# Kernel tuning notes

Hardware: AMD Instinct MI355X
Metric: run time of the kernel (lower is better)

Reference implementation:

```python
import jax, jax.numpy as jnp
import numpy as np

OBJ_DIM, REL_DIM, EFF_DIM = 3, 1, 1
REL_HID, OBJ_HID = 150, 100
B, N, E = 4, 2048, 8192
N_RECUR = 1


def _linear_init(k, fan_in, fan_out):
    s = 1.0 / np.sqrt(fan_in)
    k1, k2 = jax.random.split(k)
    W = jax.random.uniform(k1, (fan_in, fan_out), jnp.float32, -s, s)
    b = jax.random.uniform(k2, (fan_out,), jnp.float32, -s, s)
    return W, b


def setup_inputs() -> dict:
    key = jax.random.key(0)
    ks = jax.random.split(key, 9)
    objects = jax.random.normal(ks[0], (B, N, OBJ_DIM), jnp.float32)
    # one-hot incidence matrices [B, N, E]: column e selects sender/receiver node of edge e
    snd_idx = jax.random.randint(ks[1], (B, E), 0, N)
    rcv_idx = jax.random.randint(ks[2], (B, E), 0, N)
    sender_relations = jax.nn.one_hot(snd_idx, N, dtype=jnp.float32).transpose(0, 2, 1)
    receiver_relations = jax.nn.one_hot(rcv_idx, N, dtype=jnp.float32).transpose(0, 2, 1)
    relation_info = jax.random.normal(ks[3], (B, REL_DIM, E), jnp.float32)
    rW1, rb1 = _linear_init(ks[4], 2 * OBJ_DIM + REL_DIM, REL_HID)
    rW2, rb2 = _linear_init(ks[5], REL_HID, REL_HID)
    rW3, rb3 = _linear_init(ks[6], REL_HID, EFF_DIM)
    oW1, ob1 = _linear_init(ks[7], OBJ_DIM + EFF_DIM, OBJ_HID)
    oW2, ob2 = _linear_init(ks[8], OBJ_HID, OBJ_DIM)
    return dict(objects=objects, sender_relations=sender_relations,
                receiver_relations=receiver_relations, relation_info=relation_info,
                rW1=rW1, rb1=rb1, rW2=rW2, rb2=rb2, rW3=rW3, rb3=rb3,
                oW1=oW1, ob1=ob1, oW2=oW2, ob2=ob2)


def _relational(x, rW1, rb1, rW2, rb2, rW3, rb3):
    # per-edge MLP: [B, E, 2*obj+rel] -> [B, E, eff], sigmoid head (edge weight)
    h = jax.nn.relu(x @ rW1 + rb1)
    h = jax.nn.relu(h @ rW2 + rb2)
    return jax.nn.sigmoid(h @ rW3 + rb3)


def _object(x, oW1, ob1, oW2, ob2):
    # per-node MLP: [B, N, obj+eff] -> [B, N, obj]
    h = jax.nn.relu(x @ oW1 + ob1)
    return h @ oW2 + ob2


def reference(objects, sender_relations, receiver_relations, relation_info,
              rW1, rb1, rW2, rb2, rW3, rb3, oW1, ob1, oW2, ob2):
    obj = objects                                   # [B, N, D]
    rel_t = relation_info.transpose(0, 2, 1)        # [B, E, REL_DIM]
    for _ in range(N_RECUR):
        # gather via dense one-hot matmul (faithful to torch.matmul(obj.t(), S))
        snd = jnp.einsum('bnd,bne->bed', obj, sender_relations)
        rcv = jnp.einsum('bnd,bne->bed', obj, receiver_relations)
        inter = jnp.concatenate([snd, rcv, rel_t], axis=-1)      # [B, E, 2D+rel]
        eff = _relational(inter, rW1, rb1, rW2, rb2, rW3, rb3)   # [B, E, eff]
        eff_rcv = jnp.einsum('bne,bef->bnf', receiver_relations, eff)  # scatter-add to nodes
        agg = jnp.concatenate([obj, eff_rcv], axis=-1)           # [B, N, D+eff]
        obj = _object(agg, oW1, ob1, oW2, ob2)
    snd = jnp.einsum('bnd,bne->bed', obj, sender_relations)
    rcv = jnp.einsum('bnd,bne->bed', obj, receiver_relations)
    inter = jnp.concatenate([snd, rcv, rel_t], axis=-1)
    edge_weights = _relational(inter, rW1, rb1, rW2, rb2, rW3, rb3)  # [B, E, eff]
    return edge_weights
```

## Files before the change

kernel.cpp:

```cpp
#include <hip/hip_runtime.h>

#define BB 4
#define NN 2048
#define EE 8192
#define RH 150
#define RHP 152
#define LSTR 156
#define OH 100
#define JPW 19

typedef float f4_t __attribute__((ext_vector_type(4)));

__global__ __launch_bounds__(256) void extract_idx2_kernel(
    const float* __restrict__ S, const float* __restrict__ R,
    int* __restrict__ snd_idx, int* __restrict__ rcv_idx)
{
    const bool second = blockIdx.x >= 2048;
    const float* __restrict__ M = second ? R : S;
    int* __restrict__ idx = second ? rcv_idx : snd_idx;

    const unsigned total4 = (unsigned)BB * NN * EE / 4u;
    unsigned i = (blockIdx.x & 2047u) * 256u + threadIdx.x;
    const unsigned stride = 2048u * 256u;
    for (; i < total4; i += stride) {
        const f4_t v = __builtin_nontemporal_load(reinterpret_cast<const f4_t*>(M) + i);
        if (v.x > 0.5f || v.y > 0.5f || v.z > 0.5f || v.w > 0.5f) {
            const unsigned flat = i * 4u;
            const unsigned e = flat & (EE - 1u);
            const unsigned n = (flat >> 13) & (NN - 1u);
            const unsigned b = flat >> 24;
            if (v.x > 0.5f) idx[b * EE + e + 0u] = (int)n;
            if (v.y > 0.5f) idx[b * EE + e + 1u] = (int)n;
            if (v.z > 0.5f) idx[b * EE + e + 2u] = (int)n;
            if (v.w > 0.5f) idx[b * EE + e + 3u] = (int)n;
        }
    }
}

__global__ void pad_weights_kernel(const float* __restrict__ W2, const float* __restrict__ b2,
                                   const float* __restrict__ W3,
                                   float* __restrict__ W2p, float* __restrict__ b2p,
                                   float* __restrict__ W3p) {
    const int t = blockIdx.x * 256 + (int)threadIdx.x;
    if (t < RHP * RHP) {
        const int k = t / RHP, j = t - k * RHP;
        W2p[t] = (k < RH && j < RH) ? W2[k * RH + j] : 0.0f;
    }
    if (t < RHP) {
        b2p[t] = (t < RH) ? b2[t] : 0.0f;
        W3p[t] = (t < RH) ? W3[t] : 0.0f;
    }
}

template <int PASS>
__global__ __launch_bounds__(512) void edge_mlp_v3(
    const float* __restrict__ obj,
    const int* __restrict__ snd_idx, const int* __restrict__ rcv_idx,
    const float* __restrict__ rel,
    const float* __restrict__ W1, const float* __restrict__ b1,
    const float* __restrict__ W2p, const float* __restrict__ b2p,
    const float* __restrict__ W3p, const float* __restrict__ b3,
    float* __restrict__ out)
{
    __shared__ float h1s[64 * LSTR];
    __shared__ float red[512];

    const int t = (int)threadIdx.x;
    const int ebase = (int)blockIdx.x * 64;
    const int e = t & 63;
    const int jg = t >> 6;
    const int eg = ebase + e;
    const int b = eg >> 13;

    float x[7];
    {
        const int sn = snd_idx[eg];
        const int rn = rcv_idx[eg];
        const float* ps = obj + ((b << 11) + sn) * 3;
        const float* pr = obj + ((b << 11) + rn) * 3;
        x[0] = ps[0]; x[1] = ps[1]; x[2] = ps[2];
        x[3] = pr[0]; x[4] = pr[1]; x[5] = pr[2];
        x[6] = rel[eg];
    }

    for (int j = jg; j < LSTR; j += 8) {
        float v = 0.0f;
        if (j < RH) {
            v = b1[j];
#pragma unroll
            for (int k = 0; k < 7; ++k) v = fmaf(x[k], W1[k * RH + j], v);
            v = fmaxf(v, 0.0f);
        }
        h1s[e * LSTR + j] = v;
    }
    __syncthreads();

    const int w = __builtin_amdgcn_readfirstlane(jg);
    const int jbase = w * JPW;

    float acc[JPW];
#pragma unroll
    for (int m = 0; m < JPW; ++m) acc[m] = b2p[jbase + m];

    const float* hrow = h1s + e * LSTR;
    for (int kc = 0; kc < RHP; kc += 4) {
        const float4 hv = *reinterpret_cast<const float4*>(hrow + kc);
        const float* r0 = W2p + (kc + 0) * RHP + jbase;
        const float* r1 = r0 + RHP;
        const float* r2 = r1 + RHP;
        const float* r3 = r2 + RHP;
#pragma unroll
        for (int m = 0; m < JPW; ++m) {
            float a = acc[m];
            a = fmaf(hv.x, r0[m], a);
            a = fmaf(hv.y, r1[m], a);
            a = fmaf(hv.z, r2[m], a);
            a = fmaf(hv.w, r3[m], a);
            acc[m] = a;
        }
    }

    float o = 0.0f;
#pragma unroll
    for (int m = 0; m < JPW; ++m)
        o = fmaf(fmaxf(acc[m], 0.0f), W3p[jbase + m], o);

    red[t] = o;
    __syncthreads();

    if (t < 64) {
        float tot = b3[0];
#pragma unroll
        for (int i = 0; i < 8; ++i) tot += red[t + 64 * i];
        const float eff = 1.0f / (1.0f + __expf(-tot));
        if (PASS == 0) atomicAdd(&out[(b << 11) + rcv_idx[eg]], eff);
        else           out[eg] = eff;
    }
}

__global__ void object_mlp_kernel(
    const float* __restrict__ obj, const float* __restrict__ eff_rcv,
    const float* __restrict__ W1, const float* __restrict__ b1,
    const float* __restrict__ W2, const float* __restrict__ b2,
    float* __restrict__ obj_new)
{
    const int t = blockIdx.x * blockDim.x + (int)threadIdx.x;
    if (t >= BB * NN) return;
    const float x0 = obj[t * 3 + 0];
    const float x1 = obj[t * 3 + 1];
    const float x2 = obj[t * 3 + 2];
    const float x3 = eff_rcv[t];
    float a0 = b2[0], a1 = b2[1], a2 = b2[2];
#pragma unroll
    for (int j = 0; j < OH; ++j) {
        float h = b1[j];
        h = fmaf(x0, W1[0 * OH + j], h);
        h = fmaf(x1, W1[1 * OH + j], h);
        h = fmaf(x2, W1[2 * OH + j], h);
        h = fmaf(x3, W1[3 * OH + j], h);
        h = fmaxf(h, 0.0f);
        a0 = fmaf(h, W2[j * 3 + 0], a0);
        a1 = fmaf(h, W2[j * 3 + 1], a1);
        a2 = fmaf(h, W2[j * 3 + 2], a2);
    }
    obj_new[t * 3 + 0] = a0;
    obj_new[t * 3 + 1] = a1;
    obj_new[t * 3 + 2] = a2;
}

extern "C" void kernel_launch(void* const* d_in, const int* in_sizes, int n_in,
                              void* d_out, int out_size, void* d_ws, size_t ws_size,
                              hipStream_t stream) {
    (void)in_sizes; (void)n_in; (void)out_size; (void)ws_size;

    const float* objects = (const float*)d_in[0];
    const float* S       = (const float*)d_in[1];
    const float* R       = (const float*)d_in[2];
    const float* rel     = (const float*)d_in[3];
    const float* rW1     = (const float*)d_in[4];
    const float* rb1     = (const float*)d_in[5];
    const float* rW2     = (const float*)d_in[6];
    const float* rb2     = (const float*)d_in[7];
    const float* rW3     = (const float*)d_in[8];
    const float* rb3     = (const float*)d_in[9];
    const float* oW1     = (const float*)d_in[10];
    const float* ob1     = (const float*)d_in[11];
    const float* oW2     = (const float*)d_in[12];
    const float* ob2     = (const float*)d_in[13];

    char* ws = (char*)d_ws;
    int*   snd_idx = (int*)(ws + 0);
    int*   rcv_idx = (int*)(ws + (128 << 10));
    float* eff_rcv = (float*)(ws + (256 << 10));
    float* obj_new = (float*)(ws + (288 << 10));
    float* W2p     = (float*)(ws + (384 << 10));
    float* b2p     = (float*)(ws + (480 << 10));
    float* W3p     = (float*)(ws + (481 << 10));

    extract_idx2_kernel<<<4096, 256, 0, stream>>>(S, R, snd_idx, rcv_idx);

    pad_weights_kernel<<<(RHP * RHP + 255) / 256, 256, 0, stream>>>(
        rW2, rb2, rW3, W2p, b2p, W3p);
    hipMemsetAsync(eff_rcv, 0, BB * NN * sizeof(float), stream);

    edge_mlp_v3<0><<<(BB * EE) / 64, 512, 0, stream>>>(
        objects, snd_idx, rcv_idx, rel, rW1, rb1, W2p, b2p, W3p, rb3, eff_rcv);

    object_mlp_kernel<<<(BB * NN + 255) / 256, 256, 0, stream>>>(
        objects, eff_rcv, oW1, ob1, oW2, ob2, obj_new);

    edge_mlp_v3<1><<<(BB * EE) / 64, 512, 0, stream>>>(
        obj_new, snd_idx, rcv_idx, rel, rW1, rb1, W2p, b2p, W3p, rb3, (float*)d_out);
}
```

Measured before the change: 140.7 us.

## Fuse weight padding into index scan and object MLP into second edge pass

Merges the weight padding and eff_rcv zeroing into the index-extraction kernel, which removes a kernel launch and a memset. The object MLP is folded into the second edge kernel: each block recomputes the updated node features for the 128 sender and receiver nodes its edges touch, so the separate object kernel and its global round trip go away. The cost is redundant object-MLP work, since nodes referenced by many edges get recomputed in several blocks, and 128 threads run a serial 100-step loop while the rest of the block waits.

```diff
diff --git a/kernel.cpp b/kernel.cpp
--- a/kernel.cpp
+++ b/kernel.cpp
@@ -11,10 +11,26 @@
 
 typedef float f4_t __attribute__((ext_vector_type(4)));
 
-__global__ __launch_bounds__(256) void extract_idx2_kernel(
+__global__ __launch_bounds__(256) void scan_prep_kernel(
     const float* __restrict__ S, const float* __restrict__ R,
-    int* __restrict__ snd_idx, int* __restrict__ rcv_idx)
-{
+    const float* __restrict__ rW2, const float* __restrict__ rb2,
+    const float* __restrict__ rW3,
+    int* __restrict__ snd_idx, int* __restrict__ rcv_idx,
+    float* __restrict__ W2p, float* __restrict__ b2p, float* __restrict__ W3p,
+    float* __restrict__ eff_rcv)
+{
+    const unsigned gtid = blockIdx.x * 256u + threadIdx.x;
+
+    if (gtid < RHP * RHP) {
+        const int k = (int)gtid / RHP, j = (int)gtid - k * RHP;
+        W2p[gtid] = (k < RH && j < RH) ? rW2[k * RH + j] : 0.0f;
+    }
+    if (gtid < RHP) {
+        b2p[gtid] = (gtid < RH) ? rb2[gtid] : 0.0f;
+        W3p[gtid] = (gtid < RH) ? rW3[gtid] : 0.0f;
+    }
+    if (gtid < BB * NN) eff_rcv[gtid] = 0.0f;
+
     const bool second = blockIdx.x >= 2048;
     const float* __restrict__ M = second ? R : S;
     int* __restrict__ idx = second ? rcv_idx : snd_idx;
@@ -37,30 +53,72 @@
     }
 }
 
-__global__ void pad_weights_kernel(const float* __restrict__ W2, const float* __restrict__ b2,
-                                   const float* __restrict__ W3,
-                                   float* __restrict__ W2p, float* __restrict__ b2p,
-                                   float* __restrict__ W3p) {
-    const int t = blockIdx.x * 256 + (int)threadIdx.x;
-    if (t < RHP * RHP) {
-        const int k = t / RHP, j = t - k * RHP;
-        W2p[t] = (k < RH && j < RH) ? W2[k * RH + j] : 0.0f;
-    }
-    if (t < RHP) {
-        b2p[t] = (t < RH) ? b2[t] : 0.0f;
-        W3p[t] = (t < RH) ? W3[t] : 0.0f;
-    }
-}
-
-template <int PASS>
-__global__ __launch_bounds__(512) void edge_mlp_v3(
+__device__ __forceinline__ float edge_mlp_body(
+    const float x[7], int t, int e, int jg,
+    const float* __restrict__ W1, const float* __restrict__ b1,
+    const float* __restrict__ W2p, const float* __restrict__ b2p,
+    const float* __restrict__ W3p, const float* __restrict__ b3,
+    float* __restrict__ h1s, float* __restrict__ red)
+{
+    for (int j = jg; j < LSTR; j += 8) {
+        float v = 0.0f;
+        if (j < RH) {
+            v = b1[j];
+#pragma unroll
+            for (int k = 0; k < 7; ++k) v = fmaf(x[k], W1[k * RH + j], v);
+            v = fmaxf(v, 0.0f);
+        }
+        h1s[e * LSTR + j] = v;
+    }
+    __syncthreads();
+
+    const int w = __builtin_amdgcn_readfirstlane(jg);
+    const int jbase = w * JPW;
+
+    float acc[JPW];
+#pragma unroll
+    for (int m = 0; m < JPW; ++m) acc[m] = b2p[jbase + m];
+
+    const float* hrow = h1s + e * LSTR;
+    for (int kc = 0; kc < RHP; kc += 4) {
+        const float4 hv = *reinterpret_cast<const float4*>(hrow + kc);
+        const float* r0 = W2p + (kc + 0) * RHP + jbase;
+        const float* r1 = r0 + RHP;
+        const float* r2 = r1 + RHP;
+        const float* r3 = r2 + RHP;
+#pragma unroll
+        for (int m = 0; m < JPW; ++m) {
+            float a = acc[m];
+            a = fmaf(hv.x, r0[m], a);
+            a = fmaf(hv.y, r1[m], a);
+            a = fmaf(hv.z, r2[m], a);
+            a = fmaf(hv.w, r3[m], a);
+            acc[m] = a;
+        }
+    }
+
+    float o = 0.0f;
+#pragma unroll
+    for (int m = 0; m < JPW; ++m)
+        o = fmaf(fmaxf(acc[m], 0.0f), W3p[jbase + m], o);
+
+    red[t] = o;
+    __syncthreads();
+
+    float tot = b3[0];
+#pragma unroll
+    for (int i = 0; i < 8; ++i) tot += red[(t & 63) + 64 * i];
+    return 1.0f / (1.0f + __expf(-tot));
+}
+
+__global__ __launch_bounds__(512) void edge0_kernel(
     const float* __restrict__ obj,
     const int* __restrict__ snd_idx, const int* __restrict__ rcv_idx,
     const float* __restrict__ rel,
     const float* __restrict__ W1, const float* __restrict__ b1,
     const float* __restrict__ W2p, const float* __restrict__ b2p,
     const float* __restrict__ W3p, const float* __restrict__ b3,
-    float* __restrict__ out)
+    float* __restrict__ eff_rcv)
 {
     __shared__ float h1s[64 * LSTR];
     __shared__ float red[512];
@@ -83,89 +141,67 @@
         x[6] = rel[eg];
     }
 
-    for (int j = jg; j < LSTR; j += 8) {
-        float v = 0.0f;
-        if (j < RH) {
-            v = b1[j];
-#pragma unroll
-            for (int k = 0; k < 7; ++k) v = fmaf(x[k], W1[k * RH + j], v);
-            v = fmaxf(v, 0.0f);
-        }
-        h1s[e * LSTR + j] = v;
-    }
-    __syncthreads();
-
-    const int w = __builtin_amdgcn_readfirstlane(jg);
-    const int jbase = w * JPW;
-
-    float acc[JPW];
-#pragma unroll
-    for (int m = 0; m < JPW; ++m) acc[m] = b2p[jbase + m];
-
-    const float* hrow = h1s + e * LSTR;
-    for (int kc = 0; kc < RHP; kc += 4) {
-        const float4 hv = *reinterpret_cast<const float4*>(hrow + kc);
-        const float* r0 = W2p + (kc + 0) * RHP + jbase;
-        const float* r1 = r0 + RHP;
-        const float* r2 = r1 + RHP;
-        const float* r3 = r2 + RHP;
-#pragma unroll
-        for (int m = 0; m < JPW; ++m) {
-            float a = acc[m];
-            a = fmaf(hv.x, r0[m], a);
-            a = fmaf(hv.y, r1[m], a);
-            a = fmaf(hv.z, r2[m], a);
-            a = fmaf(hv.w, r3[m], a);
-            acc[m] = a;
-        }
-    }
-
-    float o = 0.0f;
-#pragma unroll
-    for (int m = 0; m < JPW; ++m)
-        o = fmaf(fmaxf(acc[m], 0.0f), W3p[jbase + m], o);
-
-    red[t] = o;
-    __syncthreads();
-
-    if (t < 64) {
-        float tot = b3[0];
-#pragma unroll
-        for (int i = 0; i < 8; ++i) tot += red[t + 64 * i];
-        const float eff = 1.0f / (1.0f + __expf(-tot));
-        if (PASS == 0) atomicAdd(&out[(b << 11) + rcv_idx[eg]], eff);
-        else           out[eg] = eff;
-    }
-}
-
-__global__ void object_mlp_kernel(
-    const float* __restrict__ obj, const float* __restrict__ eff_rcv,
+    const float eff = edge_mlp_body(x, t, e, jg, W1, b1, W2p, b2p, W3p, b3, h1s, red);
+    if (t < 64) atomicAdd(&eff_rcv[(b << 11) + rcv_idx[eg]], eff);
+}
+
+__global__ __launch_bounds__(512) void edge1_kernel(
+    const float* __restrict__ objects, const float* __restrict__ eff_rcv,
+    const int* __restrict__ snd_idx, const int* __restrict__ rcv_idx,
+    const float* __restrict__ rel,
+    const float* __restrict__ oW1, const float* __restrict__ ob1,
+    const float* __restrict__ oW2, const float* __restrict__ ob2,
     const float* __restrict__ W1, const float* __restrict__ b1,
-    const float* __restrict__ W2, const float* __restrict__ b2,
-    float* __restrict__ obj_new)
-{
-    const int t = blockIdx.x * blockDim.x + (int)threadIdx.x;
-    if (t >= BB * NN) return;
-    const float x0 = obj[t * 3 + 0];
-    const float x1 = obj[t * 3 + 1];
-    const float x2 = obj[t * 3 + 2];
-    const float x3 = eff_rcv[t];
-    float a0 = b2[0], a1 = b2[1], a2 = b2[2];
-#pragma unroll
-    for (int j = 0; j < OH; ++j) {
-        float h = b1[j];
-        h = fmaf(x0, W1[0 * OH + j], h);
-        h = fmaf(x1, W1[1 * OH + j], h);
-        h = fmaf(x2, W1[2 * OH + j], h);
-        h = fmaf(x3, W1[3 * OH + j], h);
-        h = fmaxf(h, 0.0f);
-        a0 = fmaf(h, W2[j * 3 + 0], a0);
-        a1 = fmaf(h, W2[j * 3 + 1], a1);
-        a2 = fmaf(h, W2[j * 3 + 2], a2);
-    }
-    obj_new[t * 3 + 0] = a0;
-    obj_new[t * 3 + 1] = a1;
-    obj_new[t * 3 + 2] = a2;
+    const float* __restrict__ W2p, const float* __restrict__ b2p,
+    const float* __restrict__ W3p, const float* __restrict__ b3,
+    float* __restrict__ out)
+{
+    __shared__ float h1s[64 * LSTR];
+    __shared__ float red[512];
+    __shared__ int   nds[128];
+    __shared__ float onew[128][3];
+
+    const int t = (int)threadIdx.x;
+    const int ebase = (int)blockIdx.x * 64;
+    const int e = t & 63;
+    const int jg = t >> 6;
+    const int eg = ebase + e;
+    const int b = ebase >> 13;
+
+    if (t < 64)       nds[t] = snd_idx[ebase + t];
+    else if (t < 128) nds[t] = rcv_idx[ebase + (t - 64)];
+    __syncthreads();
+
+    if (t < 128) {
+        const int node = (b << 11) + nds[t];
+        const float x0 = objects[node * 3 + 0];
+        const float x1 = objects[node * 3 + 1];
+        const float x2 = objects[node * 3 + 2];
+        const float x3 = eff_rcv[node];
+        float a0 = ob2[0], a1 = ob2[1], a2 = ob2[2];
+#pragma unroll 4
+        for (int j = 0; j < OH; ++j) {
+            float h = ob1[j];
+            h = fmaf(x0, oW1[0 * OH + j], h);
+            h = fmaf(x1, oW1[1 * OH + j], h);
+            h = fmaf(x2, oW1[2 * OH + j], h);
+            h = fmaf(x3, oW1[3 * OH + j], h);
+            h = fmaxf(h, 0.0f);
+            a0 = fmaf(h, oW2[j * 3 + 0], a0);
+            a1 = fmaf(h, oW2[j * 3 + 1], a1);
+            a2 = fmaf(h, oW2[j * 3 + 2], a2);
+        }
+        onew[t][0] = a0; onew[t][1] = a1; onew[t][2] = a2;
+    }
+    __syncthreads();
+
+    float x[7];
+    x[0] = onew[e][0];      x[1] = onew[e][1];      x[2] = onew[e][2];
+    x[3] = onew[64 + e][0]; x[4] = onew[64 + e][1]; x[5] = onew[64 + e][2];
+    x[6] = rel[eg];
+
+    const float eff = edge_mlp_body(x, t, e, jg, W1, b1, W2p, b2p, W3p, b3, h1s, red);
+    if (t < 64) out[eg] = eff;
 }
 
 extern "C" void kernel_launch(void* const* d_in, const int* in_sizes, int n_in,
@@ -192,23 +228,17 @@
     int*   snd_idx = (int*)(ws + 0);
     int*   rcv_idx = (int*)(ws + (128 << 10));
     float* eff_rcv = (float*)(ws + (256 << 10));
-    float* obj_new = (float*)(ws + (288 << 10));
-    float* W2p     = (float*)(ws + (384 << 10));
-    float* b2p     = (float*)(ws + (480 << 10));
-    float* W3p     = (float*)(ws + (481 << 10));
-
-    extract_idx2_kernel<<<4096, 256, 0, stream>>>(S, R, snd_idx, rcv_idx);
-
-    pad_weights_kernel<<<(RHP * RHP + 255) / 256, 256, 0, stream>>>(
-        rW2, rb2, rW3, W2p, b2p, W3p);
-    hipMemsetAsync(eff_rcv, 0, BB * NN * sizeof(float), stream);
-
-    edge_mlp_v3<0><<<(BB * EE) / 64, 512, 0, stream>>>(
+    float* W2p     = (float*)(ws + (288 << 10));
+    float* b2p     = (float*)(ws + (384 << 10));
+    float* W3p     = (float*)(ws + (385 << 10));
+
+    scan_prep_kernel<<<4096, 256, 0, stream>>>(
+        S, R, rW2, rb2, rW3, snd_idx, rcv_idx, W2p, b2p, W3p, eff_rcv);
+
+    edge0_kernel<<<(BB * EE) / 64, 512, 0, stream>>>(
         objects, snd_idx, rcv_idx, rel, rW1, rb1, W2p, b2p, W3p, rb3, eff_rcv);
 
-    object_mlp_kernel<<<(BB * NN + 255) / 256, 256, 0, stream>>>(
-        objects, eff_rcv, oW1, ob1, oW2, ob2, obj_new);
-
-    edge_mlp_v3<1><<<(BB * EE) / 64, 512, 0, stream>>>(
-        obj_new, snd_idx, rcv_idx, rel, rW1, rb1, W2p, b2p, W3p, rb3, (float*)d_out);
-}
+    edge1_kernel<<<(BB * EE) / 64, 512, 0, stream>>>(
+        objects, eff_rcv, snd_idx, rcv_idx, rel, oW1, ob1, oW2, ob2,
+        rW1, rb1, W2p, b2p, W3p, rb3, (float*)d_out);
+}
```

Result: faster. 136.1 us (-3.2%).
